# Kernel tuning notes

Measured on AMD Instinct MI355X. Metric: run time of the kernel, lower is better.

## Reference

```python
import jax, jax.numpy as jnp
import numpy as np

INPUT_SZ = 16
HPF = 32  # hidden_per_feat_sz
INTERACTIONS = [(0, 1), (2, 3), (4, 5), (6, 7)]
N_INT = len(INTERACTIONS)
INPUT_SIZE = INPUT_SZ + 2 * N_INT          # 24
HIDDEN = (INPUT_SZ + N_INT) * HPF          # 640
BATCH, SEQ = 128, 512

# static masks, faithful to the torch code (note: only even-indexed interactions
# get U_mask rows, exactly as the original loop `range(0, len(interactions), 2)`)
_Um = np.zeros((INPUT_SIZE, HIDDEN), np.float32)
for i in range(INPUT_SZ):
    _Um[i, i * HPF:(i + 1) * HPF] = 1
for i in range(0, N_INT, 2):
    _Um[i + INPUT_SZ, i * HPF:(i + 1) * HPF] = 1
    _Um[i + INPUT_SZ + 1, i * HPF:(i + 1) * HPF] = 1
U_MASK = jnp.asarray(_Um)
V_MASK = jnp.asarray(np.kron(np.eye(INPUT_SZ + N_INT, dtype=np.float32),
                             np.ones((HPF, HPF), np.float32)))
FEAT_SEQ = np.array(list(range(INPUT_SZ)) + [f for p in INTERACTIONS for f in p])


def setup_inputs() -> dict:
    key = jax.random.key(0)
    ks = jax.random.split(key, 13)
    stdv = 1.0 / np.sqrt(HIDDEN)
    u = lambda k, s: jax.random.uniform(k, s, jnp.float32, -stdv, stdv)
    inp = {"x": jax.random.normal(ks[0], (BATCH, SEQ, INPUT_SZ), jnp.float32)}
    names = ["i", "f", "c", "o"]
    for j, n in enumerate(names):
        inp[f"U_{n}"] = u(ks[1 + 3 * j], (INPUT_SIZE, HIDDEN))
        inp[f"V_{n}"] = u(ks[2 + 3 * j], (HIDDEN, HIDDEN))
        inp[f"b_{n}"] = u(ks[3 + 3 * j], (HIDDEN,))
    return inp


def reference(x, U_i, V_i, b_i, U_f, V_f, b_f, U_c, V_c, b_c, U_o, V_o, b_o):
    # gather masked-feature view of inputs once: [B, T, INPUT_SIZE]
    xg = x[:, :, FEAT_SEQ]
    # precompute masked, gate-concatenated weights (i|f|c|o)
    Ucat = jnp.concatenate([U_i * U_MASK, U_f * U_MASK,
                            U_c * U_MASK, U_o * U_MASK], axis=1)   # [in, 4H]
    Vcat = jnp.concatenate([V_i * V_MASK, V_f * V_MASK,
                            V_c * V_MASK, V_o * V_MASK], axis=1)   # [H, 4H]
    bcat = jnp.concatenate([b_i, b_f, b_c, b_o])                   # [4H]
    # input contribution for all timesteps in one GEMM: [B, T, 4H]
    xU = jnp.einsum('bti,ig->btg', xg, Ucat) + bcat

    h0 = jnp.zeros((x.shape[0], HIDDEN), x.dtype)
    c0 = jnp.zeros_like(h0)

    def step(carry, xu_t):
        h, c = carry
        gates = xu_t + h @ Vcat
        i_t, f_t, g_t, o_t = jnp.split(gates, 4, axis=-1)
        c = jax.nn.sigmoid(f_t) * c + jax.nn.sigmoid(i_t) * jnp.tanh(g_t)
        h = jax.nn.sigmoid(o_t) * jnp.tanh(c)
        return (h, c), h

    (h_t, c_t), hs = jax.lax.scan(step, (h0, c0), jnp.swapaxes(xU, 0, 1))
    hidden_seq = jnp.swapaxes(hs, 0, 1)  # [B, T, H]
    return hidden_seq, (h_t, c_t)
```

## Files before the change

kernel.cpp:

```cpp
#include <hip/hip_runtime.h>


#define TT 512
#define HN 640
#define BN 128

typedef float f2 __attribute__((ext_vector_type(2)));

__device__ __forceinline__ float rl(float v, int s) {
  return __int_as_float(__builtin_amdgcn_readlane(__float_as_int(v), s));
}

__global__ __attribute__((amdgpu_flat_work_group_size(64, 64),
                          amdgpu_waves_per_eu(2, 4)))
void lstm_kernel(
    const float* __restrict__ x,
    const float* __restrict__ Ui, const float* __restrict__ Vi, const float* __restrict__ bi,
    const float* __restrict__ Uf, const float* __restrict__ Vf, const float* __restrict__ bf,
    const float* __restrict__ Uc, const float* __restrict__ Vc, const float* __restrict__ bc,
    const float* __restrict__ Uo, const float* __restrict__ Vo, const float* __restrict__ bo,
    float* __restrict__ out) {
  __shared__ __align__(16) float hsh[64];

  const int unit = blockIdx.x;
  const int lane = threadIdx.x;
  const int j = unit >> 7;
  const int b = unit & 127;
  const int gp = lane >> 5;
  const int n = lane & 31;
  const int col = j * 32 + n;

  const float* UG1 = gp ? Uc : Ui;
  const float* UG2 = gp ? Uo : Uf;
  const float* VG1 = gp ? Vc : Vi;
  const float* VG2 = gp ? Vo : Vf;
  const float* bG1 = gp ? bc : bi;
  const float* bG2 = gp ? bo : bf;

  const float LOG2E = 1.44269504088896340736f;
  const float B1 = gp ? (-2.f * LOG2E) : -LOG2E;
  const float B2 = -LOG2E;
  const float Ac1 = gp ? 2.f : 1.f;
  const float Cc1 = gp ? -1.f : 0.f;

  float w11 = 0.f, w21 = 0.f, w12 = 0.f, w22 = 0.f;
  int f1 = 0, f2i = 0;
  if (j < 16) {
    f1 = f2i = j;
    w11 = UG1[j * HN + col];
    w12 = UG2[j * HN + col];
    if (j == 0) {
      w11 += UG1[16 * HN + col]; w12 += UG2[16 * HN + col];
      w21  = UG1[17 * HN + col]; w22  = UG2[17 * HN + col];
      f2i = 1;
    } else if (j == 2) {
      w11 += UG1[18 * HN + col]; w12 += UG2[18 * HN + col];
      w21  = UG1[19 * HN + col]; w22  = UG2[19 * HN + col];
      f2i = 3;
    }
  }
  const float ws11 = B1 * w11, ws21 = B1 * w21, bs1 = B1 * bG1[col];
  const float ws12 = B2 * w12, ws22 = B2 * w22, bs2 = B2 * bG2[col];

  f2 wA[16], wB[16];
#pragma unroll
  for (int kp = 0; kp < 16; ++kp) {
    wA[kp].x = B1 * VG1[(j * 32 + 2 * kp) * HN + col];
    wA[kp].y = B1 * VG1[(j * 32 + 2 * kp + 1) * HN + col];
    wB[kp].x = B2 * VG2[(j * 32 + 2 * kp) * HN + col];
    wB[kp].y = B2 * VG2[(j * 32 + 2 * kp + 1) * HN + col];
  }
#pragma unroll
  for (int kp = 0; kp < 16; ++kp) {
    asm volatile("" : "+v"(wA[kp]), "+v"(wB[kp]));
  }

  float h = 0.f, c = 0.f;
  int ob = b * TT * HN + col;
#pragma unroll 1
  for (int i = 0; i < 8; ++i) {
    const int t = i * 64 + lane;
    float xc1 = x[(b * TT + t) * 16 + f1];
    float xc2 = x[(b * TT + t) * 16 + f2i];
    asm volatile("" : "+v"(xc1), "+v"(xc2));
    for (int s = 0; s < 64; ++s) {
      const float x1 = rl(xc1, s);
      const float x2 = rl(xc2, s);
      const float sx1 = fmaf(x2, ws21, fmaf(x1, ws11, bs1));
      const float sx2 = fmaf(x2, ws22, fmaf(x1, ws12, bs2));
      hsh[lane] = h;
      __builtin_amdgcn_wave_barrier();
      f2 hp[16];
      __builtin_memcpy(hp, hsh, 128);
      __builtin_amdgcn_wave_barrier();
      f2 aA = {sx1, 0.f}, aB = {sx2, 0.f};
#pragma unroll
      for (int kp = 0; kp < 16; ++kp) {
        aA = __builtin_elementwise_fma(wA[kp], hp[kp], aA);
        aB = __builtin_elementwise_fma(wB[kp], hp[kp], aB);
      }
      const float a1 = aA.x + aA.y;
      const float a2 = aB.x + aB.y;
      const float e1 = __builtin_amdgcn_exp2f(a1);
      const float e2 = __builtin_amdgcn_exp2f(a2);
      const float g1 = fmaf(Ac1, __builtin_amdgcn_rcpf(1.f + e1), Cc1);
      const float g2 = __builtin_amdgcn_rcpf(1.f + e2);
      const float p1 = __shfl_xor(g1, 32);
      const float p2 = __shfl_xor(g2, 32);
      c = fmaf(g2, c, g1 * p1);
      const float tc = fmaf(
          2.f,
          __builtin_amdgcn_rcpf(1.f + __builtin_amdgcn_exp2f(-2.f * LOG2E * c)),
          -1.f);
      h = p2 * tc;
      if (lane < 32) out[ob] = h;
      ob += HN;
    }
  }
  if (lane < 32) {
    out[BN * TT * HN + b * HN + col] = h;
    out[BN * TT * HN + BN * HN + b * HN + col] = c;
  }
}

extern "C" void kernel_launch(void* const* d_in, const int* in_sizes, int n_in,
                              void* d_out, int out_size, void* d_ws, size_t ws_size,
                              hipStream_t stream) {
  (void)in_sizes; (void)n_in; (void)d_ws; (void)ws_size; (void)out_size;
  const float* x  = (const float*)d_in[0];
  const float* Ui = (const float*)d_in[1];
  const float* Vi = (const float*)d_in[2];
  const float* bi = (const float*)d_in[3];
  const float* Uf = (const float*)d_in[4];
  const float* Vf = (const float*)d_in[5];
  const float* bf = (const float*)d_in[6];
  const float* Uc = (const float*)d_in[7];
  const float* Vc = (const float*)d_in[8];
  const float* bc = (const float*)d_in[9];
  const float* Uo = (const float*)d_in[10];
  const float* Vo = (const float*)d_in[11];
  const float* bo = (const float*)d_in[12];
  float* out = (float*)d_out;

  dim3 grid(2560);
  dim3 block(64);
  hipLaunchKernelGGL(lstm_kernel, grid, block, 0, stream,
                     x, Ui, Vi, bi, Uf, Vf, bf, Uc, Vc, bc, Uo, Vo, bo, out);
}
```

Before: 385.0 us.

## Interleave two batch rows per wave in hand-written asm LSTM recurrence

Each wave now handles two independent batch sequences instead of one, and the grid is halved. The recurrence is written in inline assembly so that one sequence's packed-FMA matvec overlaps the other's transcendental and LDS latency chain. Weights are staged through LDS into fixed VGPRs, x values are broadcast with ds_bpermute, x loads are prefetched one chunk ahead, and outputs go through buffer stores. The cost is heavy register use, which lowers occupancy, and fragile hand-placed waitcnt/nop scheduling.

```diff
diff --git a/kernel.cpp b/kernel.cpp
--- a/kernel.cpp
+++ b/kernel.cpp
@@ -6,13 +6,9 @@
 #define BN 128
 
 typedef float f2 __attribute__((ext_vector_type(2)));
-
-__device__ __forceinline__ float rl(float v, int s) {
-  return __int_as_float(__builtin_amdgcn_readlane(__float_as_int(v), s));
-}
-
-__global__ __attribute__((amdgpu_flat_work_group_size(64, 64),
-                          amdgpu_waves_per_eu(2, 4)))
+typedef unsigned int u32x4 __attribute__((ext_vector_type(4)));
+
+__global__ __attribute__((amdgpu_flat_work_group_size(64, 64)))
 void lstm_kernel(
     const float* __restrict__ x,
     const float* __restrict__ Ui, const float* __restrict__ Vi, const float* __restrict__ bi,
@@ -20,106 +16,301 @@
     const float* __restrict__ Uc, const float* __restrict__ Vc, const float* __restrict__ bc,
     const float* __restrict__ Uo, const float* __restrict__ Vo, const float* __restrict__ bo,
     float* __restrict__ out) {
-  __shared__ __align__(16) float hsh[64];
+  __shared__ __align__(16) float lds[4480];
 
   const int unit = blockIdx.x;
   const int lane = threadIdx.x;
-  const int j = unit >> 7;
-  const int b = unit & 127;
+  const int j  = unit >> 6;
+  const int bp = unit & 63;
   const int gp = lane >> 5;
-  const int n = lane & 31;
+  const int n  = lane & 31;
   const int col = j * 32 + n;
-
-  const float* UG1 = gp ? Uc : Ui;
-  const float* UG2 = gp ? Uo : Uf;
-  const float* VG1 = gp ? Vc : Vi;
-  const float* VG2 = gp ? Vo : Vf;
-  const float* bG1 = gp ? bc : bi;
-  const float* bG2 = gp ? bo : bf;
+  const int bA = bp * 2, bB = bp * 2 + 1;
 
   const float LOG2E = 1.44269504088896340736f;
-  const float B1 = gp ? (-2.f * LOG2E) : -LOG2E;
-  const float B2 = -LOG2E;
+  const float Bs = -LOG2E;
+  const float Bg = -2.f * LOG2E;
+
+  {
+    const float* W1 = (lane < 32) ? Vi : Vc;
+    const float* W2 = (lane < 32) ? Vf : Vo;
+    const float s1 = (lane < 32) ? Bs : Bg;
+    for (int k = 0; k < 32; ++k) {
+      const int r = (j * 32 + k) * HN + col;
+      lds[lane * 68 + 2 * k]     = s1 * W1[r];
+      lds[lane * 68 + 2 * k + 1] = Bs * W2[r];
+    }
+  }
+
+  int f1 = 0, f2i = 0;
+  if (j < 16) { f1 = f2i = j; if (j == 0) f2i = 1; else if (j == 2) f2i = 3; }
+  auto uw = [&](const float* __restrict__ U, float& w1, float& w2) {
+    w1 = 0.f; w2 = 0.f;
+    if (j < 16) {
+      w1 = U[j * HN + col];
+      if (j == 0)      { w1 += U[16 * HN + col]; w2 = U[17 * HN + col]; }
+      else if (j == 2) { w1 += U[18 * HN + col]; w2 = U[19 * HN + col]; }
+    }
+  };
+  float a1w, a2w, b1w, b2w;
+  uw(gp ? Uc : Ui, a1w, a2w);
+  uw(gp ? Uo : Uf, b1w, b2w);
+  const float B1 = gp ? Bg : Bs;
+  const f2 w11P = {B1 * a1w, Bs * b1w};
+  const f2 w21P = {B1 * a2w, Bs * b2w};
+  const f2 bsP  = {B1 * (gp ? bc[col] : bi[col]), Bs * (gp ? bo[col] : bf[col])};
   const float Ac1 = gp ? 2.f : 1.f;
   const float Cc1 = gp ? -1.f : 0.f;
 
-  float w11 = 0.f, w21 = 0.f, w12 = 0.f, w22 = 0.f;
-  int f1 = 0, f2i = 0;
-  if (j < 16) {
-    f1 = f2i = j;
-    w11 = UG1[j * HN + col];
-    w12 = UG2[j * HN + col];
-    if (j == 0) {
-      w11 += UG1[16 * HN + col]; w12 += UG2[16 * HN + col];
-      w21  = UG1[17 * HN + col]; w22  = UG2[17 * HN + col];
-      f2i = 1;
-    } else if (j == 2) {
-      w11 += UG1[18 * HN + col]; w12 += UG2[18 * HN + col];
-      w21  = UG1[19 * HN + col]; w22  = UG2[19 * HN + col];
-      f2i = 3;
-    }
-  }
-  const float ws11 = B1 * w11, ws21 = B1 * w21, bs1 = B1 * bG1[col];
-  const float ws12 = B2 * w12, ws22 = B2 * w22, bs2 = B2 * bG2[col];
-
-  f2 wA[16], wB[16];
-#pragma unroll
-  for (int kp = 0; kp < 16; ++kp) {
-    wA[kp].x = B1 * VG1[(j * 32 + 2 * kp) * HN + col];
-    wA[kp].y = B1 * VG1[(j * 32 + 2 * kp + 1) * HN + col];
-    wB[kp].x = B2 * VG2[(j * 32 + 2 * kp) * HN + col];
-    wB[kp].y = B2 * VG2[(j * 32 + 2 * kp + 1) * HN + col];
-  }
-#pragma unroll
-  for (int kp = 0; kp < 16; ++kp) {
-    asm volatile("" : "+v"(wA[kp]), "+v"(wB[kp]));
-  }
-
-  float h = 0.f, c = 0.f;
-  int ob = b * TT * HN + col;
-#pragma unroll 1
-  for (int i = 0; i < 8; ++i) {
-    const int t = i * 64 + lane;
-    float xc1 = x[(b * TT + t) * 16 + f1];
-    float xc2 = x[(b * TT + t) * 16 + f2i];
-    asm volatile("" : "+v"(xc1), "+v"(xc2));
-    for (int s = 0; s < 64; ++s) {
-      const float x1 = rl(xc1, s);
-      const float x2 = rl(xc2, s);
-      const float sx1 = fmaf(x2, ws21, fmaf(x1, ws11, bs1));
-      const float sx2 = fmaf(x2, ws22, fmaf(x1, ws12, bs2));
-      hsh[lane] = h;
-      __builtin_amdgcn_wave_barrier();
-      f2 hp[16];
-      __builtin_memcpy(hp, hsh, 128);
-      __builtin_amdgcn_wave_barrier();
-      f2 aA = {sx1, 0.f}, aB = {sx2, 0.f};
-#pragma unroll
-      for (int kp = 0; kp < 16; ++kp) {
-        aA = __builtin_elementwise_fma(wA[kp], hp[kp], aA);
-        aB = __builtin_elementwise_fma(wB[kp], hp[kp], aB);
-      }
-      const float a1 = aA.x + aA.y;
-      const float a2 = aB.x + aB.y;
-      const float e1 = __builtin_amdgcn_exp2f(a1);
-      const float e2 = __builtin_amdgcn_exp2f(a2);
-      const float g1 = fmaf(Ac1, __builtin_amdgcn_rcpf(1.f + e1), Cc1);
-      const float g2 = __builtin_amdgcn_rcpf(1.f + e2);
-      const float p1 = __shfl_xor(g1, 32);
-      const float p2 = __shfl_xor(g2, 32);
-      c = fmaf(g2, c, g1 * p1);
-      const float tc = fmaf(
-          2.f,
-          __builtin_amdgcn_rcpf(1.f + __builtin_amdgcn_exp2f(-2.f * LOG2E * c)),
-          -1.f);
-      h = p2 * tc;
-      if (lane < 32) out[ob] = h;
-      ob += HN;
-    }
-  }
+  const unsigned zb = (unsigned)(unsigned long long)&lds[0];
+  const unsigned wrd    = zb + (unsigned)lane * 272u;
+  const unsigned hrdA   = zb + 17408u;
+  const unsigned hrdB   = zb + 17664u;
+  const unsigned laddrA = hrdA + (unsigned)lane * 4u;
+  const unsigned laddrB = hrdB + (unsigned)lane * 4u;
+  const unsigned swz    = (unsigned)((lane ^ 32) & 63) * 4u;
+
+  u32x4 xsrd, osrd;
+  { const unsigned long long a = (unsigned long long)x;
+    xsrd.x = (unsigned)a; xsrd.y = (unsigned)(a >> 32);
+    xsrd.z = (unsigned)(BN * TT * 16 * 4); xsrd.w = 0x00020000u; }
+  { const unsigned long long a = (unsigned long long)out;
+    osrd.x = (unsigned)a; osrd.y = (unsigned)(a >> 32);
+    osrd.z = (unsigned)((BN * TT * HN + 2 * BN * HN) * 4); osrd.w = 0x00020000u; }
+
+  unsigned voffA = (lane < 32) ? (unsigned)((bA * TT * HN + col) * 4) : 0x60000000u;
+  unsigned voffB = (lane < 32) ? (unsigned)((bB * TT * HN + col) * 4) : 0x60000000u;
+  unsigned xvA = (unsigned)(((bA * TT + lane) * 16 + f1) * 4);
+  unsigned xvB = (unsigned)(((bB * TT + lane) * 16 + f1) * 4);
+  const int sfd = (f2i - f1) * 4;
+
+  float hA = 0.f, cA = 0.f, hB = 0.f, cB = 0.f;
+
+#define AMAC(M, WE, WO, HP) \
+    "v_pk_fma_f32 v[40:41], v[" #WE "], v[" #HP "], v[40:41] op_sel:[0,0,0] op_sel_hi:[1,0,1]\n\t" \
+    "v_pk_fma_f32 v[42:43], v[" #WO "], v[" #HP "], v[42:43] op_sel:[0,1,0] op_sel_hi:[1,1,1]\n\t"
+#define BMAC(M, WE, WO, HP) \
+    "v_pk_fma_f32 v[44:45], v[" #WE "], v[" #HP "], v[44:45] op_sel:[0,0,0] op_sel_hi:[1,0,1]\n\t" \
+    "v_pk_fma_f32 v[46:47], v[" #WO "], v[" #HP "], v[46:47] op_sel:[0,1,0] op_sel_hi:[1,1,1]\n\t"
+
+  asm volatile(
+    "s_waitcnt lgkmcnt(0)\n\t"
+    "ds_read_b128 v[96:99],   %[wrd]\n\t"
+    "ds_read_b128 v[100:103], %[wrd] offset:16\n\t"
+    "ds_read_b128 v[104:107], %[wrd] offset:32\n\t"
+    "ds_read_b128 v[108:111], %[wrd] offset:48\n\t"
+    "ds_read_b128 v[112:115], %[wrd] offset:64\n\t"
+    "ds_read_b128 v[116:119], %[wrd] offset:80\n\t"
+    "ds_read_b128 v[120:123], %[wrd] offset:96\n\t"
+    "ds_read_b128 v[124:127], %[wrd] offset:112\n\t"
+    "ds_read_b128 v[128:131], %[wrd] offset:128\n\t"
+    "ds_read_b128 v[132:135], %[wrd] offset:144\n\t"
+    "ds_read_b128 v[136:139], %[wrd] offset:160\n\t"
+    "ds_read_b128 v[140:143], %[wrd] offset:176\n\t"
+    "ds_read_b128 v[144:147], %[wrd] offset:192\n\t"
+    "ds_read_b128 v[148:151], %[wrd] offset:208\n\t"
+    "ds_read_b128 v[152:155], %[wrd] offset:224\n\t"
+    "ds_read_b128 v[156:159], %[wrd] offset:240\n\t"
+    "buffer_load_dword v24, %[xvA], %[xsrd], 0 offen\n\t"
+    "buffer_load_dword v25, %[xvA], %[xsrd], %[sfd] offen\n\t"
+    "buffer_load_dword v26, %[xvB], %[xsrd], 0 offen\n\t"
+    "buffer_load_dword v27, %[xvB], %[xsrd], %[sfd] offen\n\t"
+    "v_add_u32 %[xvA], 0x1000, %[xvA]\n\t"
+    "v_add_u32 %[xvB], 0x1000, %[xvB]\n\t"
+    "buffer_load_dword v28, %[xvA], %[xsrd], 0 offen\n\t"
+    "buffer_load_dword v29, %[xvA], %[xsrd], %[sfd] offen\n\t"
+    "buffer_load_dword v30, %[xvB], %[xsrd], 0 offen\n\t"
+    "buffer_load_dword v31, %[xvB], %[xsrd], %[sfd] offen\n\t"
+    "s_waitcnt lgkmcnt(0)\n\t"
+    "ds_write_b32 %[laddrA], %[hA]\n\t"
+    "ds_read_b128 v[48:51], %[hrdA]\n\t"
+    "ds_read_b128 v[52:55], %[hrdA] offset:16\n\t"
+    "ds_read_b128 v[56:59], %[hrdA] offset:32\n\t"
+    "ds_read_b128 v[60:63], %[hrdA] offset:48\n\t"
+    "ds_read_b128 v[64:67], %[hrdA] offset:64\n\t"
+    "ds_read_b128 v[68:71], %[hrdA] offset:80\n\t"
+    "ds_read_b128 v[72:75], %[hrdA] offset:96\n\t"
+    "ds_read_b128 v[76:79], %[hrdA] offset:112\n\t"
+    "ds_write_b32 %[laddrB], %[hB]\n\t"
+    "ds_read_b128 v[160:163], %[hrdB]\n\t"
+    "ds_read_b128 v[164:167], %[hrdB] offset:16\n\t"
+    "ds_read_b128 v[168:171], %[hrdB] offset:32\n\t"
+    "ds_read_b128 v[172:175], %[hrdB] offset:48\n\t"
+    "ds_read_b128 v[176:179], %[hrdB] offset:64\n\t"
+    "ds_read_b128 v[180:183], %[hrdB] offset:80\n\t"
+    "ds_read_b128 v[184:187], %[hrdB] offset:96\n\t"
+    "ds_read_b128 v[188:191], %[hrdB] offset:112\n\t"
+    "v_mov_b32 v33, 0\n\t"
+    "s_mov_b32 s21, 8\n\t"
+    "s_waitcnt vmcnt(4)\n\t"
+    "Louter%=:\n\t"
+    "s_mov_b32 s20, 64\n\t"
+    "Lbody%=:\n\t"
+    "s_waitcnt lgkmcnt(9)\n\t"
+    "ds_bpermute_b32 v88, v33, v24\n\t"
+    "ds_bpermute_b32 v89, v33, v25\n\t"
+    "v_pk_mul_f32 v[40:41], v[96:97], v[48:49] op_sel:[0,0] op_sel_hi:[1,0]\n\t"
+    "v_pk_mul_f32 v[42:43], v[98:99], v[48:49] op_sel:[0,1] op_sel_hi:[1,1]\n\t"
+    AMAC(1,  100:101, 102:103, 50:51)
+    AMAC(2,  104:105, 106:107, 52:53)
+    AMAC(3,  108:109, 110:111, 54:55)
+    AMAC(4,  112:113, 114:115, 56:57)
+    AMAC(5,  116:117, 118:119, 58:59)
+    AMAC(6,  120:121, 122:123, 60:61)
+    AMAC(7,  124:125, 126:127, 62:63)
+    AMAC(8,  128:129, 130:131, 64:65)
+    AMAC(9,  132:133, 134:135, 66:67)
+    AMAC(10, 136:137, 138:139, 68:69)
+    AMAC(11, 140:141, 142:143, 70:71)
+    AMAC(12, 144:145, 146:147, 72:73)
+    AMAC(13, 148:149, 150:151, 74:75)
+    AMAC(14, 152:153, 154:155, 76:77)
+    AMAC(15, 156:157, 158:159, 78:79)
+    "s_waitcnt lgkmcnt(0)\n\t"
+    "v_pk_fma_f32 v[92:93], v[88:89], %[w11P], %[bsP] op_sel:[0,0,0] op_sel_hi:[0,1,1]\n\t"
+    "v_pk_fma_f32 v[92:93], v[88:89], %[w21P], v[92:93] op_sel:[1,0,0] op_sel_hi:[1,1,1]\n\t"
+    "v_pk_add_f32 v[40:41], v[40:41], v[92:93]\n\t"
+    "v_pk_add_f32 v[40:41], v[40:41], v[42:43]\n\t"
+    "v_exp_f32 v80, v40\n\t"
+    "v_exp_f32 v81, v41\n\t"
+    "v_add_f32 v80, 1.0, v80\n\t"
+    "v_add_f32 v81, 1.0, v81\n\t"
+    "v_rcp_f32 v80, v80\n\t"
+    "v_rcp_f32 v81, v81\n\t"
+    "s_nop 1\n\t"
+    "v_fma_f32 v80, %[ac1], v80, %[cc1]\n\t"
+    "ds_bpermute_b32 v82, %[swz], v80\n\t"
+    "ds_bpermute_b32 v83, %[swz], v81\n\t"
+    "ds_bpermute_b32 v90, v33, v26\n\t"
+    "ds_bpermute_b32 v91, v33, v27\n\t"
+    "v_add_u32 v33, 4, v33\n\t"
+    "v_pk_mul_f32 v[44:45], v[96:97], v[160:161] op_sel:[0,0] op_sel_hi:[1,0]\n\t"
+    "v_pk_mul_f32 v[46:47], v[98:99], v[160:161] op_sel:[0,1] op_sel_hi:[1,1]\n\t"
+    BMAC(1,  100:101, 102:103, 162:163)
+    BMAC(2,  104:105, 106:107, 164:165)
+    BMAC(3,  108:109, 110:111, 166:167)
+    BMAC(4,  112:113, 114:115, 168:169)
+    BMAC(5,  116:117, 118:119, 170:171)
+    BMAC(6,  120:121, 122:123, 172:173)
+    BMAC(7,  124:125, 126:127, 174:175)
+    BMAC(8,  128:129, 130:131, 176:177)
+    BMAC(9,  132:133, 134:135, 178:179)
+    BMAC(10, 136:137, 138:139, 180:181)
+    BMAC(11, 140:141, 142:143, 182:183)
+    BMAC(12, 144:145, 146:147, 184:185)
+    BMAC(13, 148:149, 150:151, 186:187)
+    BMAC(14, 152:153, 154:155, 188:189)
+    BMAC(15, 156:157, 158:159, 190:191)
+    "s_waitcnt lgkmcnt(0)\n\t"
+    "v_pk_fma_f32 v[92:93], v[90:91], %[w11P], %[bsP] op_sel:[0,0,0] op_sel_hi:[0,1,1]\n\t"
+    "v_pk_fma_f32 v[92:93], v[90:91], %[w21P], v[92:93] op_sel:[1,0,0] op_sel_hi:[1,1,1]\n\t"
+    "v_pk_add_f32 v[44:45], v[44:45], v[92:93]\n\t"
+    "v_pk_add_f32 v[44:45], v[44:45], v[46:47]\n\t"
+    "v_mul_f32 v92, v80, v82\n\t"
+    "v_fma_f32 %[cA], v81, %[cA], v92\n\t"
+    "v_exp_f32 v84, v44\n\t"
+    "v_exp_f32 v85, v45\n\t"
+    "v_mul_f32 v93, 0xc038aa3b, %[cA]\n\t"
+    "v_exp_f32 v93, v93\n\t"
+    "v_add_f32 v84, 1.0, v84\n\t"
+    "v_add_f32 v85, 1.0, v85\n\t"
+    "v_add_f32 v93, 1.0, v93\n\t"
+    "v_rcp_f32 v84, v84\n\t"
+    "v_rcp_f32 v85, v85\n\t"
+    "v_rcp_f32 v93, v93\n\t"
+    "s_nop 1\n\t"
+    "v_fma_f32 v84, %[ac1], v84, %[cc1]\n\t"
+    "ds_bpermute_b32 v86, %[swz], v84\n\t"
+    "ds_bpermute_b32 v87, %[swz], v85\n\t"
+    "v_fma_f32 v93, 2.0, v93, -1.0\n\t"
+    "v_mul_f32 %[hA], v83, v93\n\t"
+    "buffer_store_dword %[hA], %[voffA], %[osrd], 0 offen\n\t"
+    "v_add_u32 %[voffA], 0xa00, %[voffA]\n\t"
+    "ds_write_b32 %[laddrA], %[hA]\n\t"
+    "ds_read_b128 v[48:51], %[hrdA]\n\t"
+    "ds_read_b128 v[52:55], %[hrdA] offset:16\n\t"
+    "ds_read_b128 v[56:59], %[hrdA] offset:32\n\t"
+    "ds_read_b128 v[60:63], %[hrdA] offset:48\n\t"
+    "ds_read_b128 v[64:67], %[hrdA] offset:64\n\t"
+    "ds_read_b128 v[68:71], %[hrdA] offset:80\n\t"
+    "ds_read_b128 v[72:75], %[hrdA] offset:96\n\t"
+    "ds_read_b128 v[76:79], %[hrdA] offset:112\n\t"
+    "s_waitcnt lgkmcnt(9)\n\t"
+    "v_mul_f32 v92, v84, v86\n\t"
+    "v_fma_f32 %[cB], v85, %[cB], v92\n\t"
+    "v_mul_f32 v93, 0xc038aa3b, %[cB]\n\t"
+    "v_exp_f32 v93, v93\n\t"
+    "s_nop 1\n\t"
+    "v_add_f32 v93, 1.0, v93\n\t"
+    "v_rcp_f32 v93, v93\n\t"
+    "s_nop 1\n\t"
+    "v_fma_f32 v93, 2.0, v93, -1.0\n\t"
+    "v_mul_f32 %[hB], v87, v93\n\t"
+    "buffer_store_dword %[hB], %[voffB], %[osrd], 0 offen\n\t"
+    "v_add_u32 %[voffB], 0xa00, %[voffB]\n\t"
+    "ds_write_b32 %[laddrB], %[hB]\n\t"
+    "ds_read_b128 v[160:163], %[hrdB]\n\t"
+    "ds_read_b128 v[164:167], %[hrdB] offset:16\n\t"
+    "ds_read_b128 v[168:171], %[hrdB] offset:32\n\t"
+    "ds_read_b128 v[172:175], %[hrdB] offset:48\n\t"
+    "ds_read_b128 v[176:179], %[hrdB] offset:64\n\t"
+    "ds_read_b128 v[180:183], %[hrdB] offset:80\n\t"
+    "ds_read_b128 v[184:187], %[hrdB] offset:96\n\t"
+    "ds_read_b128 v[188:191], %[hrdB] offset:112\n\t"
+    "s_sub_u32 s20, s20, 1\n\t"
+    "s_cmp_lg_u32 s20, 0\n\t"
+    "s_cbranch_scc1 Lbody%=\n\t"
+    "s_waitcnt vmcnt(0)\n\t"
+    "v_mov_b32 v24, v28\n\t"
+    "v_mov_b32 v25, v29\n\t"
+    "v_mov_b32 v26, v30\n\t"
+    "v_mov_b32 v27, v31\n\t"
+    "v_add_u32 %[xvA], 0x1000, %[xvA]\n\t"
+    "v_add_u32 %[xvB], 0x1000, %[xvB]\n\t"
+    "buffer_load_dword v28, %[xvA], %[xsrd], 0 offen\n\t"
+    "buffer_load_dword v29, %[xvA], %[xsrd], %[sfd] offen\n\t"
+    "buffer_load_dword v30, %[xvB], %[xsrd], 0 offen\n\t"
+    "buffer_load_dword v31, %[xvB], %[xsrd], %[sfd] offen\n\t"
+    "v_mov_b32 v33, 0\n\t"
+    "s_sub_u32 s21, s21, 1\n\t"
+    "s_cmp_lg_u32 s21, 0\n\t"
+    "s_cbranch_scc1 Louter%=\n\t"
+    : [hA]"+v"(hA), [cA]"+v"(cA), [hB]"+v"(hB), [cB]"+v"(cB),
+      [voffA]"+v"(voffA), [voffB]"+v"(voffB), [xvA]"+v"(xvA), [xvB]"+v"(xvB)
+    : [wrd]"v"(wrd), [laddrA]"v"(laddrA), [hrdA]"v"(hrdA),
+      [laddrB]"v"(laddrB), [hrdB]"v"(hrdB), [swz]"v"(swz),
+      [w11P]"v"(w11P), [w21P]"v"(w21P), [bsP]"v"(bsP),
+      [ac1]"v"(Ac1), [cc1]"v"(Cc1),
+      [xsrd]"s"(xsrd), [osrd]"s"(osrd), [sfd]"s"(sfd)
+    : "memory", "scc", "s20", "s21",
+      "v24","v25","v26","v27","v28","v29","v30","v31","v33",
+      "v40","v41","v42","v43","v44","v45","v46","v47",
+      "v48","v49","v50","v51","v52","v53","v54","v55",
+      "v56","v57","v58","v59","v60","v61","v62","v63",
+      "v64","v65","v66","v67","v68","v69","v70","v71",
+      "v72","v73","v74","v75","v76","v77","v78","v79",
+      "v80","v81","v82","v83","v84","v85","v86","v87",
+      "v88","v89","v90","v91","v92","v93",
+      "v96","v97","v98","v99","v100","v101","v102","v103",
+      "v104","v105","v106","v107","v108","v109","v110","v111",
+      "v112","v113","v114","v115","v116","v117","v118","v119",
+      "v120","v121","v122","v123","v124","v125","v126","v127",
+      "v128","v129","v130","v131","v132","v133","v134","v135",
+      "v136","v137","v138","v139","v140","v141","v142","v143",
+      "v144","v145","v146","v147","v148","v149","v150","v151",
+      "v152","v153","v154","v155","v156","v157","v158","v159",
+      "v160","v161","v162","v163","v164","v165","v166","v167",
+      "v168","v169","v170","v171","v172","v173","v174","v175",
+      "v176","v177","v178","v179","v180","v181","v182","v183",
+      "v184","v185","v186","v187","v188","v189","v190","v191");
+#undef AMAC
+#undef BMAC
+
   if (lane < 32) {
-    out[BN * TT * HN + b * HN + col] = h;
-    out[BN * TT * HN + BN * HN + b * HN + col] = c;
+    out[BN * TT * HN + bA * HN + col] = hA;
+    out[BN * TT * HN + BN * HN + bA * HN + col] = cA;
+    out[BN * TT * HN + bB * HN + col] = hB;
+    out[BN * TT * HN + BN * HN + bB * HN + col] = cB;
   }
 }
 
@@ -142,7 +333,7 @@
   const float* bo = (const float*)d_in[12];
   float* out = (float*)d_out;
 
-  dim3 grid(2560);
+  dim3 grid(1280);
   dim3 block(64);
   hipLaunchKernelGGL(lstm_kernel, grid, block, 0, stream,
                      x, Ui, Vi, bi, Uf, Vf, bf, Uc, Vc, bc, Uo, Vo, bo, out);
```

Measured after the change: 435.2 us. +13.0%, slower.

## Rewrite LSTM recurrence loop in inline assembly with SGPR broadcast of h

Applied to the files above, without the earlier changes.

Replaces the compiler-generated per-timestep loop with a hand-written inline assembly loop. Hidden state is broadcast through v_readlane into scalar registers instead of an LDS round trip. Weights are staged through LDS into fixed VGPRs, and x is prefetched one chunk ahead via buffer loads. Gate exchange uses ds_bpermute, and stores use buffer_store with an out-of-range offset for the inactive half, which avoids branching. This targets the LDS write/read latency on the serial recurrence critical path, at the cost of fragile hardcoded registers, 32 serial readlanes per step, and a dropped waves_per_eu hint.

```diff
diff --git a/kernel.cpp b/kernel.cpp
--- a/kernel.cpp
+++ b/kernel.cpp
@@ -5,14 +5,9 @@
 #define HN 640
 #define BN 128
 
-typedef float f2 __attribute__((ext_vector_type(2)));
-
-__device__ __forceinline__ float rl(float v, int s) {
-  return __int_as_float(__builtin_amdgcn_readlane(__float_as_int(v), s));
-}
-
-__global__ __attribute__((amdgpu_flat_work_group_size(64, 64),
-                          amdgpu_waves_per_eu(2, 4)))
+typedef unsigned int u32x4 __attribute__((ext_vector_type(4)));
+
+__global__ __attribute__((amdgpu_flat_work_group_size(64, 64)))
 void lstm_kernel(
     const float* __restrict__ x,
     const float* __restrict__ Ui, const float* __restrict__ Vi, const float* __restrict__ bi,
@@ -20,7 +15,7 @@
     const float* __restrict__ Uc, const float* __restrict__ Vc, const float* __restrict__ bc,
     const float* __restrict__ Uo, const float* __restrict__ Vo, const float* __restrict__ bo,
     float* __restrict__ out) {
-  __shared__ __align__(16) float hsh[64];
+  __shared__ __align__(16) float lds[4352];
 
   const int unit = blockIdx.x;
   const int lane = threadIdx.x;
@@ -30,93 +25,231 @@
   const int n = lane & 31;
   const int col = j * 32 + n;
 
-  const float* UG1 = gp ? Uc : Ui;
-  const float* UG2 = gp ? Uo : Uf;
-  const float* VG1 = gp ? Vc : Vi;
-  const float* VG2 = gp ? Vo : Vf;
-  const float* bG1 = gp ? bc : bi;
-  const float* bG2 = gp ? bo : bf;
-
   const float LOG2E = 1.44269504088896340736f;
-  const float B1 = gp ? (-2.f * LOG2E) : -LOG2E;
-  const float B2 = -LOG2E;
+  const float Bs = -LOG2E;
+  const float Bg = -2.f * LOG2E;
+  const float B1 = gp ? Bg : Bs;
+
+  {
+    const float* W1 = gp ? Vc : Vi;
+    const float* W2 = gp ? Vo : Vf;
+    for (int k = 0; k < 32; ++k) {
+      const int r = (j * 32 + k) * HN + col;
+      lds[lane * 68 + k]      = B1 * W1[r];
+      lds[lane * 68 + 32 + k] = Bs * W2[r];
+    }
+  }
+
+  int f1 = 0, f2i = 0;
+  if (j < 16) { f1 = f2i = j; if (j == 0) f2i = 1; else if (j == 2) f2i = 3; }
+  auto uw = [&](const float* __restrict__ U, float& w1, float& w2) {
+    w1 = 0.f; w2 = 0.f;
+    if (j < 16) {
+      w1 = U[j * HN + col];
+      if (j == 0)      { w1 += U[16 * HN + col]; w2 = U[17 * HN + col]; }
+      else if (j == 2) { w1 += U[18 * HN + col]; w2 = U[19 * HN + col]; }
+    }
+  };
+  float a1w, a2w, b1w, b2w;
+  uw(gp ? Uc : Ui, a1w, a2w);
+  uw(gp ? Uo : Uf, b1w, b2w);
+  const float ws11 = B1 * a1w, ws21 = B1 * a2w;
+  const float bs1  = B1 * (gp ? bc[col] : bi[col]);
+  const float ws12 = Bs * b1w, ws22 = Bs * b2w;
+  const float bs2  = Bs * (gp ? bo[col] : bf[col]);
   const float Ac1 = gp ? 2.f : 1.f;
   const float Cc1 = gp ? -1.f : 0.f;
 
-  float w11 = 0.f, w21 = 0.f, w12 = 0.f, w22 = 0.f;
-  int f1 = 0, f2i = 0;
-  if (j < 16) {
-    f1 = f2i = j;
-    w11 = UG1[j * HN + col];
-    w12 = UG2[j * HN + col];
-    if (j == 0) {
-      w11 += UG1[16 * HN + col]; w12 += UG2[16 * HN + col];
-      w21  = UG1[17 * HN + col]; w22  = UG2[17 * HN + col];
-      f2i = 1;
-    } else if (j == 2) {
-      w11 += UG1[18 * HN + col]; w12 += UG2[18 * HN + col];
-      w21  = UG1[19 * HN + col]; w22  = UG2[19 * HN + col];
-      f2i = 3;
-    }
-  }
-  const float ws11 = B1 * w11, ws21 = B1 * w21, bs1 = B1 * bG1[col];
-  const float ws12 = B2 * w12, ws22 = B2 * w22, bs2 = B2 * bG2[col];
-
-  f2 wA[16], wB[16];
-#pragma unroll
-  for (int kp = 0; kp < 16; ++kp) {
-    wA[kp].x = B1 * VG1[(j * 32 + 2 * kp) * HN + col];
-    wA[kp].y = B1 * VG1[(j * 32 + 2 * kp + 1) * HN + col];
-    wB[kp].x = B2 * VG2[(j * 32 + 2 * kp) * HN + col];
-    wB[kp].y = B2 * VG2[(j * 32 + 2 * kp + 1) * HN + col];
-  }
-#pragma unroll
-  for (int kp = 0; kp < 16; ++kp) {
-    asm volatile("" : "+v"(wA[kp]), "+v"(wB[kp]));
-  }
+  const unsigned zb  = (unsigned)(unsigned long long)&lds[0];
+  const unsigned wrd = zb + (unsigned)lane * 272u;
+  const unsigned swz = (unsigned)((lane ^ 32) & 63) * 4u;
+
+  u32x4 xsrd, osrd;
+  { const unsigned long long a = (unsigned long long)x;
+    xsrd.x = (unsigned)a; xsrd.y = (unsigned)(a >> 32);
+    xsrd.z = (unsigned)(BN * TT * 16 * 4); xsrd.w = 0x00020000u; }
+  { const unsigned long long a = (unsigned long long)out;
+    osrd.x = (unsigned)a; osrd.y = (unsigned)(a >> 32);
+    osrd.z = (unsigned)((BN * TT * HN + 2 * BN * HN) * 4); osrd.w = 0x00020000u; }
+
+  unsigned voff = (lane < 32) ? (unsigned)((b * TT * HN + col) * 4)
+                              : 0x60000000u;
+  unsigned xv = (unsigned)(((b * TT + lane) * 16 + f1) * 4);
+  const int sfd = (f2i - f1) * 4;
 
   float h = 0.f, c = 0.f;
-  int ob = b * TT * HN + col;
-#pragma unroll 1
-  for (int i = 0; i < 8; ++i) {
-    const int t = i * 64 + lane;
-    float xc1 = x[(b * TT + t) * 16 + f1];
-    float xc2 = x[(b * TT + t) * 16 + f2i];
-    asm volatile("" : "+v"(xc1), "+v"(xc2));
-    for (int s = 0; s < 64; ++s) {
-      const float x1 = rl(xc1, s);
-      const float x2 = rl(xc2, s);
-      const float sx1 = fmaf(x2, ws21, fmaf(x1, ws11, bs1));
-      const float sx2 = fmaf(x2, ws22, fmaf(x1, ws12, bs2));
-      hsh[lane] = h;
-      __builtin_amdgcn_wave_barrier();
-      f2 hp[16];
-      __builtin_memcpy(hp, hsh, 128);
-      __builtin_amdgcn_wave_barrier();
-      f2 aA = {sx1, 0.f}, aB = {sx2, 0.f};
-#pragma unroll
-      for (int kp = 0; kp < 16; ++kp) {
-        aA = __builtin_elementwise_fma(wA[kp], hp[kp], aA);
-        aB = __builtin_elementwise_fma(wB[kp], hp[kp], aB);
-      }
-      const float a1 = aA.x + aA.y;
-      const float a2 = aB.x + aB.y;
-      const float e1 = __builtin_amdgcn_exp2f(a1);
-      const float e2 = __builtin_amdgcn_exp2f(a2);
-      const float g1 = fmaf(Ac1, __builtin_amdgcn_rcpf(1.f + e1), Cc1);
-      const float g2 = __builtin_amdgcn_rcpf(1.f + e2);
-      const float p1 = __shfl_xor(g1, 32);
-      const float p2 = __shfl_xor(g2, 32);
-      c = fmaf(g2, c, g1 * p1);
-      const float tc = fmaf(
-          2.f,
-          __builtin_amdgcn_rcpf(1.f + __builtin_amdgcn_exp2f(-2.f * LOG2E * c)),
-          -1.f);
-      h = p2 * tc;
-      if (lane < 32) out[ob] = h;
-      ob += HN;
-    }
-  }
+
+  asm volatile(
+    "s_waitcnt lgkmcnt(0)\n\t"
+    "ds_read_b128 v[96:99],   %[wrd]\n\t"
+    "ds_read_b128 v[100:103], %[wrd] offset:16\n\t"
+    "ds_read_b128 v[104:107], %[wrd] offset:32\n\t"
+    "ds_read_b128 v[108:111], %[wrd] offset:48\n\t"
+    "ds_read_b128 v[112:115], %[wrd] offset:64\n\t"
+    "ds_read_b128 v[116:119], %[wrd] offset:80\n\t"
+    "ds_read_b128 v[120:123], %[wrd] offset:96\n\t"
+    "ds_read_b128 v[124:127], %[wrd] offset:112\n\t"
+    "ds_read_b128 v[128:131], %[wrd] offset:128\n\t"
+    "ds_read_b128 v[132:135], %[wrd] offset:144\n\t"
+    "ds_read_b128 v[136:139], %[wrd] offset:160\n\t"
+    "ds_read_b128 v[140:143], %[wrd] offset:176\n\t"
+    "ds_read_b128 v[144:147], %[wrd] offset:192\n\t"
+    "ds_read_b128 v[148:151], %[wrd] offset:208\n\t"
+    "ds_read_b128 v[152:155], %[wrd] offset:224\n\t"
+    "ds_read_b128 v[156:159], %[wrd] offset:240\n\t"
+    "buffer_load_dword v24, %[xv], %[xsrd], 0 offen\n\t"
+    "buffer_load_dword v25, %[xv], %[xsrd], %[sfd] offen\n\t"
+    "v_add_u32 %[xv], 0x1000, %[xv]\n\t"
+    "buffer_load_dword v28, %[xv], %[xsrd], 0 offen\n\t"
+    "buffer_load_dword v29, %[xv], %[xsrd], %[sfd] offen\n\t"
+    "s_waitcnt lgkmcnt(0)\n\t"
+    "s_waitcnt vmcnt(2)\n\t"
+    "s_mov_b32 s21, 8\n\t"
+    "Louter%=:\n\t"
+    "s_mov_b32 s25, 0\n\t"
+    "s_mov_b32 s20, 64\n\t"
+    "Lbody%=:\n\t"
+    "v_readlane_b32 s26, v24, s25\n\t"
+    "v_readlane_b32 s27, v25, s25\n\t"
+    "s_add_u32 s25, s25, 1\n\t"
+    "v_readlane_b32 s40, %[h], 0\n\t"
+    "v_readlane_b32 s41, %[h], 1\n\t"
+    "v_readlane_b32 s42, %[h], 2\n\t"
+    "v_readlane_b32 s43, %[h], 3\n\t"
+    "v_readlane_b32 s44, %[h], 4\n\t"
+    "v_readlane_b32 s45, %[h], 5\n\t"
+    "v_readlane_b32 s46, %[h], 6\n\t"
+    "v_readlane_b32 s47, %[h], 7\n\t"
+    "v_readlane_b32 s48, %[h], 8\n\t"
+    "v_readlane_b32 s49, %[h], 9\n\t"
+    "v_readlane_b32 s50, %[h], 10\n\t"
+    "v_readlane_b32 s51, %[h], 11\n\t"
+    "v_readlane_b32 s52, %[h], 12\n\t"
+    "v_readlane_b32 s53, %[h], 13\n\t"
+    "v_readlane_b32 s54, %[h], 14\n\t"
+    "v_readlane_b32 s55, %[h], 15\n\t"
+    "v_readlane_b32 s56, %[h], 16\n\t"
+    "v_readlane_b32 s57, %[h], 17\n\t"
+    "v_readlane_b32 s58, %[h], 18\n\t"
+    "v_readlane_b32 s59, %[h], 19\n\t"
+    "v_readlane_b32 s60, %[h], 20\n\t"
+    "v_readlane_b32 s61, %[h], 21\n\t"
+    "v_readlane_b32 s62, %[h], 22\n\t"
+    "v_readlane_b32 s63, %[h], 23\n\t"
+    "v_readlane_b32 s64, %[h], 24\n\t"
+    "v_readlane_b32 s65, %[h], 25\n\t"
+    "v_readlane_b32 s66, %[h], 26\n\t"
+    "v_readlane_b32 s67, %[h], 27\n\t"
+    "v_readlane_b32 s68, %[h], 28\n\t"
+    "v_readlane_b32 s69, %[h], 29\n\t"
+    "v_readlane_b32 s70, %[h], 30\n\t"
+    "v_readlane_b32 s71, %[h], 31\n\t"
+    "v_mov_b32 v36, %[bs1]\n\t"
+    "v_fmac_f32 v36, s26, %[w11]\n\t"
+    "v_fmac_f32 v36, s27, %[w21]\n\t"
+    "v_mov_b32 v37, %[bs2]\n\t"
+    "v_fmac_f32 v37, s26, %[w12]\n\t"
+    "v_fmac_f32 v37, s27, %[w22]\n\t"
+    "v_mov_b32 v40, v36\n\t"
+    "v_mov_b32 v41, 0\n\t"
+    "v_mov_b32 v44, v37\n\t"
+    "v_mov_b32 v45, 0\n\t"
+    "v_pk_fma_f32 v[40:41], v[96:97],   s[40:41], v[40:41]\n\t"
+    "v_pk_fma_f32 v[44:45], v[128:129], s[40:41], v[44:45]\n\t"
+    "v_pk_mul_f32 v[42:43], v[98:99],   s[42:43]\n\t"
+    "v_pk_mul_f32 v[46:47], v[130:131], s[42:43]\n\t"
+    "v_pk_fma_f32 v[40:41], v[100:101], s[44:45], v[40:41]\n\t"
+    "v_pk_fma_f32 v[44:45], v[132:133], s[44:45], v[44:45]\n\t"
+    "v_pk_fma_f32 v[42:43], v[102:103], s[46:47], v[42:43]\n\t"
+    "v_pk_fma_f32 v[46:47], v[134:135], s[46:47], v[46:47]\n\t"
+    "v_pk_fma_f32 v[40:41], v[104:105], s[48:49], v[40:41]\n\t"
+    "v_pk_fma_f32 v[44:45], v[136:137], s[48:49], v[44:45]\n\t"
+    "v_pk_fma_f32 v[42:43], v[106:107], s[50:51], v[42:43]\n\t"
+    "v_pk_fma_f32 v[46:47], v[138:139], s[50:51], v[46:47]\n\t"
+    "v_pk_fma_f32 v[40:41], v[108:109], s[52:53], v[40:41]\n\t"
+    "v_pk_fma_f32 v[44:45], v[140:141], s[52:53], v[44:45]\n\t"
+    "v_pk_fma_f32 v[42:43], v[110:111], s[54:55], v[42:43]\n\t"
+    "v_pk_fma_f32 v[46:47], v[142:143], s[54:55], v[46:47]\n\t"
+    "v_pk_fma_f32 v[40:41], v[112:113], s[56:57], v[40:41]\n\t"
+    "v_pk_fma_f32 v[44:45], v[144:145], s[56:57], v[44:45]\n\t"
+    "v_pk_fma_f32 v[42:43], v[114:115], s[58:59], v[42:43]\n\t"
+    "v_pk_fma_f32 v[46:47], v[146:147], s[58:59], v[46:47]\n\t"
+    "v_pk_fma_f32 v[40:41], v[116:117], s[60:61], v[40:41]\n\t"
+    "v_pk_fma_f32 v[44:45], v[148:149], s[60:61], v[44:45]\n\t"
+    "v_pk_fma_f32 v[42:43], v[118:119], s[62:63], v[42:43]\n\t"
+    "v_pk_fma_f32 v[46:47], v[150:151], s[62:63], v[46:47]\n\t"
+    "v_pk_fma_f32 v[40:41], v[120:121], s[64:65], v[40:41]\n\t"
+    "v_pk_fma_f32 v[44:45], v[152:153], s[64:65], v[44:45]\n\t"
+    "v_pk_fma_f32 v[42:43], v[122:123], s[66:67], v[42:43]\n\t"
+    "v_pk_fma_f32 v[46:47], v[154:155], s[66:67], v[46:47]\n\t"
+    "v_pk_fma_f32 v[40:41], v[124:125], s[68:69], v[40:41]\n\t"
+    "v_pk_fma_f32 v[44:45], v[156:157], s[68:69], v[44:45]\n\t"
+    "v_pk_fma_f32 v[42:43], v[126:127], s[70:71], v[42:43]\n\t"
+    "v_pk_fma_f32 v[46:47], v[158:159], s[70:71], v[46:47]\n\t"
+    "v_pk_add_f32 v[40:41], v[40:41], v[42:43]\n\t"
+    "v_pk_add_f32 v[44:45], v[44:45], v[46:47]\n\t"
+    "v_add_f32 v80, v40, v41\n\t"
+    "v_add_f32 v81, v44, v45\n\t"
+    "v_exp_f32 v80, v80\n\t"
+    "v_exp_f32 v81, v81\n\t"
+    "s_nop 1\n\t"
+    "v_add_f32 v80, 1.0, v80\n\t"
+    "v_add_f32 v81, 1.0, v81\n\t"
+    "v_rcp_f32 v80, v80\n\t"
+    "v_rcp_f32 v81, v81\n\t"
+    "s_nop 1\n\t"
+    "v_fma_f32 v80, %[ac1], v80, %[cc1]\n\t"
+    "ds_bpermute_b32 v82, %[swz], v80\n\t"
+    "ds_bpermute_b32 v83, %[swz], v81\n\t"
+    "s_waitcnt lgkmcnt(0)\n\t"
+    "v_mul_f32 v84, v80, v82\n\t"
+    "v_fma_f32 %[c], v81, %[c], v84\n\t"
+    "v_mul_f32 v85, 0xc038aa3b, %[c]\n\t"
+    "v_exp_f32 v85, v85\n\t"
+    "s_nop 1\n\t"
+    "v_add_f32 v85, 1.0, v85\n\t"
+    "v_rcp_f32 v85, v85\n\t"
+    "s_nop 1\n\t"
+    "v_fma_f32 v85, 2.0, v85, -1.0\n\t"
+    "v_mul_f32 %[h], v83, v85\n\t"
+    "buffer_store_dword %[h], %[voff], %[osrd], 0 offen\n\t"
+    "v_add_u32 %[voff], 0xa00, %[voff]\n\t"
+    "s_sub_u32 s20, s20, 1\n\t"
+    "s_cmp_lg_u32 s20, 0\n\t"
+    "s_cbranch_scc1 Lbody%=\n\t"
+    "s_waitcnt vmcnt(0)\n\t"
+    "v_mov_b32 v24, v28\n\t"
+    "v_mov_b32 v25, v29\n\t"
+    "v_add_u32 %[xv], 0x1000, %[xv]\n\t"
+    "buffer_load_dword v28, %[xv], %[xsrd], 0 offen\n\t"
+    "buffer_load_dword v29, %[xv], %[xsrd], %[sfd] offen\n\t"
+    "s_sub_u32 s21, s21, 1\n\t"
+    "s_cmp_lg_u32 s21, 0\n\t"
+    "s_cbranch_scc1 Louter%=\n\t"
+    : [h]"+v"(h), [c]"+v"(c), [voff]"+v"(voff), [xv]"+v"(xv)
+    : [wrd]"v"(wrd), [swz]"v"(swz),
+      [w11]"v"(ws11), [w21]"v"(ws21), [bs1]"v"(bs1),
+      [w12]"v"(ws12), [w22]"v"(ws22), [bs2]"v"(bs2),
+      [ac1]"v"(Ac1), [cc1]"v"(Cc1),
+      [xsrd]"s"(xsrd), [osrd]"s"(osrd), [sfd]"s"(sfd)
+    : "memory", "scc",
+      "s20","s21","s25","s26","s27",
+      "s40","s41","s42","s43","s44","s45","s46","s47",
+      "s48","s49","s50","s51","s52","s53","s54","s55",
+      "s56","s57","s58","s59","s60","s61","s62","s63",
+      "s64","s65","s66","s67","s68","s69","s70","s71",
+      "v24","v25","v28","v29","v36","v37",
+      "v40","v41","v42","v43","v44","v45","v46","v47",
+      "v80","v81","v82","v83","v84","v85",
+      "v96","v97","v98","v99","v100","v101","v102","v103",
+      "v104","v105","v106","v107","v108","v109","v110","v111",
+      "v112","v113","v114","v115","v116","v117","v118","v119",
+      "v120","v121","v122","v123","v124","v125","v126","v127",
+      "v128","v129","v130","v131","v132","v133","v134","v135",
+      "v136","v137","v138","v139","v140","v141","v142","v143",
+      "v144","v145","v146","v147","v148","v149","v150","v151",
+      "v152","v153","v154","v155","v156","v157","v158","v159");
+
   if (lane < 32) {
     out[BN * TT * HN + b * HN + col] = h;
     out[BN * TT * HN + BN * HN + b * HN + col] = c;
```

After: 564.2 us. 1.47x slower.
